# Optimization experiments

Hardware: AMD Instinct MI355X
Metric: run time of the kernel (lower is better)

The kernel has to match this reference:

```python
import jax, jax.numpy as jnp
import numpy as np

B, S, V, E, H, T = 256, 160, 50000, 300, 256, 200

def setup_inputs() -> dict:
    key = jax.random.key(0)
    ks = jax.random.split(key, 12)
    return {
        'x1': jax.random.randint(ks[0], (B, S), 0, V),
        'x2': jax.random.randint(ks[1], (B, S), 0, V),
        'x1mask': jnp.ones((B, S), jnp.float32),
        'key_c': jax.random.normal(ks[2], (B, S, T), jnp.float32) * 0.1,
        'key_r': jax.random.normal(ks[3], (B, S, T), jnp.float32) * 0.1,
        'emb_table': jax.random.normal(ks[4], (V, E), jnp.float32) * 0.1,
        'W_ih': jax.random.normal(ks[5], (4 * H, E), jnp.float32) * 0.05,
        'W_hh': jax.random.normal(ks[6], (4 * H, H), jnp.float32) * 0.05,
        'W_kh': jax.random.normal(ks[7], (4 * H, T), jnp.float32) * 0.05,
        'b_g': jnp.zeros((4 * H,), jnp.float32),
        'W_attn': jax.random.normal(ks[8], (H, H), jnp.float32) * 0.05,
        'b_attn': jnp.zeros((H,), jnp.float32),
        'M': jax.random.normal(ks[9], (H, H), jnp.float32) * 0.05,
        'b': jnp.zeros((1,), jnp.float32),
    }

def _run_rnn(x_emb, k_emb, W_ih, W_hh, W_kh, b_g):
    # x_emb: [B,S,E], k_emb: [B,S,T] -> hidden states [B,S,H]
    Bn = x_emb.shape[0]
    h0 = jnp.zeros((Bn, H), x_emb.dtype)
    c0 = jnp.zeros((Bn, H), x_emb.dtype)
    def cell(carry, inp):
        h, c = carry
        x_t, k_t = inp
        g = x_t @ W_ih.T + h @ W_hh.T + k_t @ W_kh.T + b_g  # [B,4H]
        i, f, gg, o = jnp.split(g, 4, axis=-1)
        c = jax.nn.sigmoid(f) * c + jax.nn.sigmoid(i) * jnp.tanh(gg)
        h = jax.nn.sigmoid(o) * jnp.tanh(c)
        return (h, c), h
    xs = (jnp.swapaxes(x_emb, 0, 1), jnp.swapaxes(k_emb, 0, 1))  # time-major
    (_, _), hs = jax.lax.scan(cell, (h0, c0), xs)
    return jnp.swapaxes(hs, 0, 1)  # [B,S,H]

def reference(x1, x2, x1mask, key_c, key_r, emb_table, W_ih, W_hh, W_kh, b_g,
              W_attn, b_attn, M, b):
    x1_emb = emb_table[x1]  # [B,S,E] (dropout = identity at eval)
    x2_emb = emb_table[x2]
    sc = _run_rnn(x1_emb, key_c, W_ih, W_hh, W_kh, b_g)  # context states [B,S,H]
    rs = _run_rnn(x2_emb, key_r, W_ih, W_hh, W_kh, b_g)
    r = rs[:, -1]  # last response hidden [B,H]
    # masked dot-product attention over context states keyed by r
    attn = sc @ W_attn.T + b_attn  # [B,S,H]
    energies = jnp.einsum('bsh,bh->bs', attn, r) * x1mask
    alpha = jax.nn.softmax(energies, axis=-1)
    c_attn = jnp.einsum('bs,bsh->bh', alpha, sc)
    # bilinear score
    o = jnp.einsum('bh,hk,bk->b', c_attn, M, r) + b[0]
    return o
```

## Files before the change

kernel.cpp:

```cpp
#include <hip/hip_runtime.h>
#include <math.h>

#define B_   256
#define S_   160
#define E_   300
#define H_   256
#define T_   200
#define G4H  1024
#define CH   16
#define NCH  10

typedef float  f32x4  __attribute__((ext_vector_type(4)));
typedef __bf16 bf16x4 __attribute__((ext_vector_type(4)));
typedef __bf16 bf16x8 __attribute__((ext_vector_type(8)));

__device__ __forceinline__ float sigf(float x) {
    float e = expf(-fabsf(x));
    float p = 1.0f / (1.0f + e);
    return x >= 0.0f ? p : e * p;
}

__device__ __forceinline__ int norig(int np) {
    return ((np >> 4) & 3) * 256 + ((np >> 6) << 4) + (np & 15);
}

__device__ __forceinline__ float4 pick4(const float* __restrict__ e,
                                        const float* __restrict__ k, int kg) {
    if (kg < E_)      return *(const float4*)(e + kg);
    if (kg < E_ + T_) return *(const float4*)(k + (kg - E_));
    return make_float4(0.f, 0.f, 0.f, 0.f);
}

__device__ __forceinline__ void split4(float4 v, bf16x4& h, bf16x4& l) {
    h[0] = (__bf16)v.x; l[0] = (__bf16)(v.x - (float)h[0]);
    h[1] = (__bf16)v.y; l[1] = (__bf16)(v.y - (float)h[1]);
    h[2] = (__bf16)v.z; l[2] = (__bf16)(v.z - (float)h[2]);
    h[3] = (__bf16)v.w; l[3] = (__bf16)(v.w - (float)h[3]);
}

__global__ __launch_bounds__(128) void prep_split(
    const float* __restrict__ Whh, const float* __restrict__ Wih,
    const float* __restrict__ Wkh,
    __bf16* __restrict__ whh_hi, __bf16* __restrict__ whh_lo,
    __bf16* __restrict__ wik_hi, __bf16* __restrict__ wik_lo)
{
    const int n  = blockIdx.x;
    const int np = ((n & 255) >> 4) * 64 + (n >> 8) * 16 + (n & 15);
    const int t  = threadIdx.x;
    {
        const int k4 = t * 4;
        float4 v;
        if (k4 < E_)            v = *(const float4*)(Wih + (size_t)n * E_ + k4);
        else if (k4 < E_ + T_)  v = *(const float4*)(Wkh + (size_t)n * T_ + (k4 - E_));
        else                    v = make_float4(0.f, 0.f, 0.f, 0.f);
        bf16x4 h, l;
        split4(v, h, l);
        *(bf16x4*)(wik_hi + (size_t)np * 512 + k4) = h;
        *(bf16x4*)(wik_lo + (size_t)np * 512 + k4) = l;
    }
    if (t < 64) {
        const int k4 = t * 4;
        const float4 v = *(const float4*)(Whh + (size_t)n * 256 + k4);
        bf16x4 h, l;
        split4(v, h, l);
        *(bf16x4*)(whh_hi + (size_t)np * 256 + k4) = h;
        *(bf16x4*)(whh_lo + (size_t)np * 256 + k4) = l;
    }
}

__global__ __launch_bounds__(256, 4) void gemm_g2(
    const int* __restrict__ x1, const int* __restrict__ x2,
    const float* __restrict__ key_c, const float* __restrict__ key_r,
    const float* __restrict__ emb,
    const __bf16* __restrict__ wik_hi, const __bf16* __restrict__ wik_lo,
    const float* __restrict__ bg,
    float* __restrict__ G, int s0)
{
    __shared__ __align__(16) __bf16 Ah[128 * 32];
    __shared__ __align__(16) __bf16 Al[128 * 32];
    __shared__ __align__(16) __bf16 Bh[128 * 32];
    __shared__ __align__(16) __bf16 Bl[128 * 32];

    const int t   = threadIdx.x;
    const int rnn = blockIdx.z;
    const int m0  = blockIdx.x * 128;
    const int n0  = blockIdx.y * 128;
    const int* xx = rnn ? x2 : x1;
    const float* key = rnn ? key_r : key_c;

    const int r0  = t >> 3;
    const int kq  = t & 7;
    const int csw = (((kq >> 1) ^ ((r0 >> 1) & 3)) * 16) + (kq & 1) * 8;

    const float* aeb[4]; const float* akb[4];
    const __bf16* wph[4]; const __bf16* wpl[4];
    #pragma unroll
    for (int i = 0; i < 4; ++i) {
        const int row = r0 + 32 * i;
        const int am  = m0 + row;
        const int bs  = (am >> 4) * S_ + s0 + (am & 15);
        aeb[i] = emb + (size_t)xx[bs] * E_;
        akb[i] = key + (size_t)bs * T_;
        wph[i] = wik_hi + (size_t)(n0 + row) * 512;
        wpl[i] = wik_lo + (size_t)(n0 + row) * 512;
    }

    const int w  = t >> 6;
    const int wm = w >> 1;
    const int wn = w & 1;
    const int l  = t & 63;
    const int cl = l & 15;
    const int ch = l >> 4;
    const int chs = ((ch ^ ((cl >> 1) & 3)) * 16);

    f32x4 acc[4][4];
    #pragma unroll
    for (int fm = 0; fm < 4; ++fm)
        #pragma unroll
        for (int fn = 0; fn < 4; ++fn) acc[fm][fn] = (f32x4){0.f, 0.f, 0.f, 0.f};

    for (int kt = 0; kt < 16; ++kt) {
        const int kg = kt * 32 + kq * 4;
        bf16x4 sAh[4], sAl[4], sBh[4], sBl[4];
        #pragma unroll
        for (int i = 0; i < 4; ++i) {
            const float4 va = pick4(aeb[i], akb[i], kg);
            split4(va, sAh[i], sAl[i]);
            sBh[i] = *(const bf16x4*)(wph[i] + kg);
            sBl[i] = *(const bf16x4*)(wpl[i] + kg);
        }
        __syncthreads();
        #pragma unroll
        for (int i = 0; i < 4; ++i) {
            const int off = (r0 + 32 * i) * 64 + csw;
            *(bf16x4*)((char*)Ah + off) = sAh[i];
            *(bf16x4*)((char*)Al + off) = sAl[i];
            *(bf16x4*)((char*)Bh + off) = sBh[i];
            *(bf16x4*)((char*)Bl + off) = sBl[i];
        }
        __syncthreads();

        bf16x8 fBh[4], fBl[4];
        #pragma unroll
        for (int fn = 0; fn < 4; ++fn) {
            const int off = (wn * 64 + fn * 16 + cl) * 64 + chs;
            fBh[fn] = *(const bf16x8*)((const char*)Bh + off);
            fBl[fn] = *(const bf16x8*)((const char*)Bl + off);
        }
        #pragma unroll
        for (int fm = 0; fm < 4; ++fm) {
            const int off = (wm * 64 + fm * 16 + cl) * 64 + chs;
            const bf16x8 fAh = *(const bf16x8*)((const char*)Ah + off);
            const bf16x8 fAl = *(const bf16x8*)((const char*)Al + off);
            #pragma unroll
            for (int fn = 0; fn < 4; ++fn) {
                acc[fm][fn] = __builtin_amdgcn_mfma_f32_16x16x32_bf16(fAh, fBh[fn], acc[fm][fn], 0, 0, 0);
                acc[fm][fn] = __builtin_amdgcn_mfma_f32_16x16x32_bf16(fAh, fBl[fn], acc[fm][fn], 0, 0, 0);
                acc[fm][fn] = __builtin_amdgcn_mfma_f32_16x16x32_bf16(fAl, fBh[fn], acc[fm][fn], 0, 0, 0);
            }
        }
    }

    float bgl[4];
    #pragma unroll
    for (int fn = 0; fn < 4; ++fn) bgl[fn] = bg[norig(n0 + wn * 64 + fn * 16 + cl)];

    #pragma unroll
    for (int fm = 0; fm < 4; ++fm) {
        #pragma unroll
        for (int r = 0; r < 4; ++r) {
            const int m  = m0 + wm * 64 + fm * 16 + ch * 4 + r;
            const int b  = m >> 4;
            const int sl = m & 15;
            float* rowp = G + ((size_t)(rnn * CH + sl) * B_ + b) * G4H;
            #pragma unroll
            for (int fn = 0; fn < 4; ++fn)
                rowp[n0 + wn * 64 + fn * 16 + cl] = acc[fm][fn][r] + bgl[fn];
        }
    }
}

__global__ __launch_bounds__(256, 2) void lstm_ks(
    const float* __restrict__ G,
    const __bf16* __restrict__ Whi, const __bf16* __restrict__ Wlo,
    const __bf16* __restrict__ hhi_in, const __bf16* __restrict__ hlo_in,
    __bf16* __restrict__ hhi_out, __bf16* __restrict__ hlo_out,
    float* __restrict__ cst, float* __restrict__ sc,
    int sl, int s_glob, int first)
{
    __shared__ float ps[64 * 66];

    const int t  = threadIdx.x;
    const int w  = t >> 6;
    const int l  = t & 63;
    const int cl = l & 15;
    const int ch = l >> 4;
    const int mt = blockIdx.x;
    const int jt = blockIdx.y;
    const int rnn = mt >> 4;
    const int b0  = (mt & 15) * 16;
    const int m0  = mt * 16;

    const int me = t >> 4;
    const int jl = t & 15;
    const int j  = jt * 16 + jl;
    float Ge[4];
    const float* Gb = G + ((size_t)(rnn * CH + sl) * B_ + b0 + me) * G4H + jt * 64;
    #pragma unroll
    for (int g = 0; g < 4; ++g) Ge[g] = Gb[g * 16 + jl];
    const float c_in = first ? 0.f : cst[(size_t)(m0 + me) * 256 + j];

    const size_t ab = (size_t)(m0 + cl) * 256 + w * 64 + ch * 8;
    const bf16x8 fAh0 = *(const bf16x8*)(hhi_in + ab);
    const bf16x8 fAh1 = *(const bf16x8*)(hhi_in + ab + 32);
    const bf16x8 fAl0 = *(const bf16x8*)(hlo_in + ab);
    const bf16x8 fAl1 = *(const bf16x8*)(hlo_in + ab + 32);

    bf16x8 fBh[4][2], fBl[4][2];
    #pragma unroll
    for (int g = 0; g < 4; ++g) {
        const size_t bb = (size_t)(jt * 64 + g * 16 + cl) * 256 + w * 64 + ch * 8;
        fBh[g][0] = *(const bf16x8*)(Whi + bb);
        fBh[g][1] = *(const bf16x8*)(Whi + bb + 32);
        fBl[g][0] = *(const bf16x8*)(Wlo + bb);
        fBl[g][1] = *(const bf16x8*)(Wlo + bb + 32);
    }

    f32x4 acc[4];
    #pragma unroll
    for (int g = 0; g < 4; ++g) acc[g] = (f32x4){0.f, 0.f, 0.f, 0.f};
    #pragma unroll
    for (int g = 0; g < 4; ++g) {
        acc[g] = __builtin_amdgcn_mfma_f32_16x16x32_bf16(fAh0, fBh[g][0], acc[g], 0, 0, 0);
        acc[g] = __builtin_amdgcn_mfma_f32_16x16x32_bf16(fAh1, fBh[g][1], acc[g], 0, 0, 0);
        acc[g] = __builtin_amdgcn_mfma_f32_16x16x32_bf16(fAh0, fBl[g][0], acc[g], 0, 0, 0);
        acc[g] = __builtin_amdgcn_mfma_f32_16x16x32_bf16(fAh1, fBl[g][1], acc[g], 0, 0, 0);
        acc[g] = __builtin_amdgcn_mfma_f32_16x16x32_bf16(fAl0, fBh[g][0], acc[g], 0, 0, 0);
        acc[g] = __builtin_amdgcn_mfma_f32_16x16x32_bf16(fAl1, fBh[g][1], acc[g], 0, 0, 0);
    }

    #pragma unroll
    for (int g = 0; g < 4; ++g)
        #pragma unroll
        for (int r = 0; r < 4; ++r)
            ps[(w * 16 + ch * 4 + r) * 66 + g * 16 + cl] = acc[g][r];
    __syncthreads();

    float g4[4];
    #pragma unroll
    for (int g = 0; g < 4; ++g) {
        float s = Ge[g];
        #pragma unroll
        for (int w2 = 0; w2 < 4; ++w2)
            s += ps[(w2 * 16 + me) * 66 + g * 16 + jl];
        g4[g] = s;
    }
    const float c = sigf(g4[1]) * c_in + sigf(g4[0]) * tanhf(g4[2]);
    const float h = sigf(g4[3]) * tanhf(c);
    cst[(size_t)(m0 + me) * 256 + j] = c;
    const __bf16 hh = (__bf16)h;
    const size_t ho = (size_t)(m0 + me) * 256 + j;
    hhi_out[ho] = hh;
    hlo_out[ho] = (__bf16)(h - (float)hh);
    if (rnn == 0)
        sc[((size_t)(b0 + me) * S_ + s_glob) * H_ + j] = h;
}

__global__ __launch_bounds__(256) void final_kernel(
    const float* __restrict__ sc,
    const __bf16* __restrict__ rhi, const __bf16* __restrict__ rlo,
    const float* __restrict__ Wattn, const float* __restrict__ battn,
    const float* __restrict__ M, const float* __restrict__ bscal,
    const float* __restrict__ mask, float* __restrict__ out)
{
    __shared__ float rs[256], us[256], red[256], as_[256];
    const int b = blockIdx.x;
    const int t = threadIdx.x;

    const size_t ri = (size_t)(256 + b) * 256 + t;
    rs[t] = (float)rhi[ri] + (float)rlo[ri];
    __syncthreads();

    float acc = 0.0f;
    for (int h = 0; h < 256; ++h) acc += rs[h] * Wattn[h * 256 + t];
    us[t] = acc;

    red[t] = battn[t] * rs[t];
    __syncthreads();
    for (int off = 128; off; off >>= 1) {
        if (t < off) red[t] += red[t + off];
        __syncthreads();
    }
    float beta = red[0];
    __syncthreads();

    float vh = 0.0f;
    {
        const float* Mrow = M + t * 256;
        for (int k = 0; k < 256; ++k) vh += Mrow[k] * rs[k];
    }

    float e = -INFINITY;
    if (t < S_) {
        float d = 0.0f;
        const float* scrow = sc + ((size_t)b * S_ + t) * H_;
        for (int h = 0; h < 256; ++h) d += scrow[h] * us[h];
        e = (d + beta) * mask[b * S_ + t];
    }
    red[t] = e;
    __syncthreads();
    for (int off = 128; off; off >>= 1) {
        if (t < off) red[t] = fmaxf(red[t], red[t + off]);
        __syncthreads();
    }
    float mx = red[0];
    __syncthreads();

    float p = (t < S_) ? expf(e - mx) : 0.0f;
    as_[t] = p;
    red[t] = p;
    __syncthreads();
    for (int off = 128; off; off >>= 1) {
        if (t < off) red[t] += red[t + off];
        __syncthreads();
    }
    float inv = 1.0f / red[0];
    __syncthreads();

    float ca = 0.0f;
    for (int s = 0; s < S_; ++s) ca += as_[s] * sc[((size_t)b * S_ + s) * H_ + t];
    ca *= inv;

    red[t] = ca * vh;
    __syncthreads();
    for (int off = 128; off; off >>= 1) {
        if (t < off) red[t] += red[t + off];
        __syncthreads();
    }
    if (t == 0) out[b] = red[0] + bscal[0];
}

extern "C" void kernel_launch(void* const* d_in, const int* in_sizes, int n_in,
                              void* d_out, int out_size, void* d_ws, size_t ws_size,
                              hipStream_t stream)
{
    const int*   x1    = (const int*)d_in[0];
    const int*   x2    = (const int*)d_in[1];
    const float* mask  = (const float*)d_in[2];
    const float* key_c = (const float*)d_in[3];
    const float* key_r = (const float*)d_in[4];
    const float* emb   = (const float*)d_in[5];
    const float* Wih   = (const float*)d_in[6];
    const float* Whh   = (const float*)d_in[7];
    const float* Wkh   = (const float*)d_in[8];
    const float* bg    = (const float*)d_in[9];
    const float* Wattn = (const float*)d_in[10];
    const float* battn = (const float*)d_in[11];
    const float* M     = (const float*)d_in[12];
    const float* bb    = (const float*)d_in[13];
    float* out = (float*)d_out;
    char*  wsb = (char*)d_ws;

    float*  G     = (float*)(wsb + 0);
    float*  sc    = (float*)(wsb + 33554432);
    __bf16* hhi0  = (__bf16*)(wsb + 75497472);
    __bf16* hlo0  = (__bf16*)(wsb + 75759616);
    __bf16* hhi1  = (__bf16*)(wsb + 76021760);
    __bf16* hlo1  = (__bf16*)(wsb + 76283904);
    float*  cst   = (float*)(wsb + 76546048);
    __bf16* WhhHi = (__bf16*)(wsb + 77070336);
    __bf16* WhhLo = (__bf16*)(wsb + 77594624);
    __bf16* WikHi = (__bf16*)(wsb + 78118912);
    __bf16* WikLo = (__bf16*)(wsb + 79167488);
    if (ws_size < 80216064) return;

    hipMemsetAsync(hhi0, 0, 524288, stream);
    prep_split<<<dim3(1024), 128, 0, stream>>>(Whh, Wih, Wkh,
                                               WhhHi, WhhLo, WikHi, WikLo);

    for (int ci = 0; ci < NCH; ++ci) {
        gemm_g2<<<dim3(32, 8, 2), 256, 0, stream>>>(x1, x2, key_c, key_r, emb,
                                                    WikHi, WikLo, bg, G, ci * CH);
        for (int slq = 0; slq < CH; ++slq) {
            const int s   = ci * CH + slq;
            const int par = s & 1;
            lstm_ks<<<dim3(32, 16), 256, 0, stream>>>(G, WhhHi, WhhLo,
                                                      par ? hhi1 : hhi0,
                                                      par ? hlo1 : hlo0,
                                                      par ? hhi0 : hhi1,
                                                      par ? hlo0 : hlo1,
                                                      cst, sc, slq, s, s == 0);
        }
    }

    final_kernel<<<dim3(256), 256, 0, stream>>>(sc, hhi0, hlo0, Wattn, battn,
                                                M, bb, mask, out);
}
```

Measured before the change: 1.603 ms.

## Double threads per block in input GEMM and LSTM step kernels

Both the chunked input-projection GEMM and the per-step recurrent LSTM kernel now launch 512 threads per block instead of 256. In the GEMM, each wave covers a 64x32 output subtile and each thread stages one row with 8-wide loads. In the LSTM step, the K=256 reduction is split across 8 waves of 32 instead of 4 waves of 64, with a larger shared partial-sum buffer, and only the first 256 threads run the gate nonlinearities. The aim is more waves in flight and shorter per-wave MFMA chains on the latency-bound recurrent step, at the cost of more shared-memory reduction work and half the threads idling in the epilogue.

```diff
diff --git a/kernel.cpp b/kernel.cpp
--- a/kernel.cpp
+++ b/kernel.cpp
@@ -68,7 +68,7 @@
     }
 }
 
-__global__ __launch_bounds__(256, 4) void gemm_g2(
+__global__ __launch_bounds__(512, 2) void gemm_g2(
     const int* __restrict__ x1, const int* __restrict__ x2,
     const float* __restrict__ key_c, const float* __restrict__ key_r,
     const float* __restrict__ emb,
@@ -88,62 +88,60 @@
     const int* xx = rnn ? x2 : x1;
     const float* key = rnn ? key_r : key_c;
 
-    const int r0  = t >> 3;
-    const int kq  = t & 7;
-    const int csw = (((kq >> 1) ^ ((r0 >> 1) & 3)) * 16) + (kq & 1) * 8;
-
-    const float* aeb[4]; const float* akb[4];
-    const __bf16* wph[4]; const __bf16* wpl[4];
-    #pragma unroll
-    for (int i = 0; i < 4; ++i) {
-        const int row = r0 + 32 * i;
-        const int am  = m0 + row;
-        const int bs  = (am >> 4) * S_ + s0 + (am & 15);
-        aeb[i] = emb + (size_t)xx[bs] * E_;
-        akb[i] = key + (size_t)bs * T_;
-        wph[i] = wik_hi + (size_t)(n0 + row) * 512;
-        wpl[i] = wik_lo + (size_t)(n0 + row) * 512;
+    const int r0 = t >> 2;
+    const int cq = t & 3;
+    const int csw = ((cq ^ ((r0 >> 1) & 3)) * 16);
+
+    const float* aeb; const float* akb;
+    const __bf16* wph; const __bf16* wpl;
+    {
+        const int am = m0 + r0;
+        const int bs = (am >> 4) * S_ + s0 + (am & 15);
+        aeb = emb + (size_t)xx[bs] * E_;
+        akb = key + (size_t)bs * T_;
+        wph = wik_hi + (size_t)(n0 + r0) * 512;
+        wpl = wik_lo + (size_t)(n0 + r0) * 512;
     }
 
     const int w  = t >> 6;
-    const int wm = w >> 1;
-    const int wn = w & 1;
+    const int wm = w >> 2;
+    const int wn = w & 3;
     const int l  = t & 63;
     const int cl = l & 15;
     const int ch = l >> 4;
     const int chs = ((ch ^ ((cl >> 1) & 3)) * 16);
 
-    f32x4 acc[4][4];
+    f32x4 acc[4][2];
     #pragma unroll
     for (int fm = 0; fm < 4; ++fm)
         #pragma unroll
-        for (int fn = 0; fn < 4; ++fn) acc[fm][fn] = (f32x4){0.f, 0.f, 0.f, 0.f};
+        for (int fn = 0; fn < 2; ++fn) acc[fm][fn] = (f32x4){0.f, 0.f, 0.f, 0.f};
 
     for (int kt = 0; kt < 16; ++kt) {
-        const int kg = kt * 32 + kq * 4;
-        bf16x4 sAh[4], sAl[4], sBh[4], sBl[4];
-        #pragma unroll
-        for (int i = 0; i < 4; ++i) {
-            const float4 va = pick4(aeb[i], akb[i], kg);
-            split4(va, sAh[i], sAl[i]);
-            sBh[i] = *(const bf16x4*)(wph[i] + kg);
-            sBl[i] = *(const bf16x4*)(wpl[i] + kg);
-        }
-        __syncthreads();
-        #pragma unroll
-        for (int i = 0; i < 4; ++i) {
-            const int off = (r0 + 32 * i) * 64 + csw;
-            *(bf16x4*)((char*)Ah + off) = sAh[i];
-            *(bf16x4*)((char*)Al + off) = sAl[i];
-            *(bf16x4*)((char*)Bh + off) = sBh[i];
-            *(bf16x4*)((char*)Bl + off) = sBl[i];
-        }
-        __syncthreads();
-
-        bf16x8 fBh[4], fBl[4];
-        #pragma unroll
-        for (int fn = 0; fn < 4; ++fn) {
-            const int off = (wn * 64 + fn * 16 + cl) * 64 + chs;
+        const int kg = kt * 32 + cq * 8;
+        const float4 va0 = pick4(aeb, akb, kg);
+        const float4 va1 = pick4(aeb, akb, kg + 4);
+        const bf16x8 vbh = *(const bf16x8*)(wph + kg);
+        const bf16x8 vbl = *(const bf16x8*)(wpl + kg);
+        bf16x4 h0, l0, h1, l1;
+        split4(va0, h0, l0);
+        split4(va1, h1, l1);
+        const bf16x8 sah = __builtin_shufflevector(h0, h1, 0, 1, 2, 3, 4, 5, 6, 7);
+        const bf16x8 sal = __builtin_shufflevector(l0, l1, 0, 1, 2, 3, 4, 5, 6, 7);
+        __syncthreads();
+        {
+            const int off = r0 * 64 + csw;
+            *(bf16x8*)((char*)Ah + off) = sah;
+            *(bf16x8*)((char*)Al + off) = sal;
+            *(bf16x8*)((char*)Bh + off) = vbh;
+            *(bf16x8*)((char*)Bl + off) = vbl;
+        }
+        __syncthreads();
+
+        bf16x8 fBh[2], fBl[2];
+        #pragma unroll
+        for (int fn = 0; fn < 2; ++fn) {
+            const int off = (wn * 32 + fn * 16 + cl) * 64 + chs;
             fBh[fn] = *(const bf16x8*)((const char*)Bh + off);
             fBl[fn] = *(const bf16x8*)((const char*)Bl + off);
         }
@@ -153,7 +151,7 @@
             const bf16x8 fAh = *(const bf16x8*)((const char*)Ah + off);
             const bf16x8 fAl = *(const bf16x8*)((const char*)Al + off);
             #pragma unroll
-            for (int fn = 0; fn < 4; ++fn) {
+            for (int fn = 0; fn < 2; ++fn) {
                 acc[fm][fn] = __builtin_amdgcn_mfma_f32_16x16x32_bf16(fAh, fBh[fn], acc[fm][fn], 0, 0, 0);
                 acc[fm][fn] = __builtin_amdgcn_mfma_f32_16x16x32_bf16(fAh, fBl[fn], acc[fm][fn], 0, 0, 0);
                 acc[fm][fn] = __builtin_amdgcn_mfma_f32_16x16x32_bf16(fAl, fBh[fn], acc[fm][fn], 0, 0, 0);
@@ -161,9 +159,10 @@
         }
     }
 
-    float bgl[4];
-    #pragma unroll
-    for (int fn = 0; fn < 4; ++fn) bgl[fn] = bg[norig(n0 + wn * 64 + fn * 16 + cl)];
+    float bgl[2];
+    #pragma unroll
+    for (int fn = 0; fn < 2; ++fn)
+        bgl[fn] = bg[norig(n0 + wn * 32 + fn * 16 + cl)];
 
     #pragma unroll
     for (int fm = 0; fm < 4; ++fm) {
@@ -174,13 +173,13 @@
             const int sl = m & 15;
             float* rowp = G + ((size_t)(rnn * CH + sl) * B_ + b) * G4H;
             #pragma unroll
-            for (int fn = 0; fn < 4; ++fn)
-                rowp[n0 + wn * 64 + fn * 16 + cl] = acc[fm][fn][r] + bgl[fn];
-        }
-    }
-}
-
-__global__ __launch_bounds__(256, 2) void lstm_ks(
+            for (int fn = 0; fn < 2; ++fn)
+                rowp[n0 + wn * 32 + fn * 16 + cl] = acc[fm][fn][r] + bgl[fn];
+        }
+    }
+}
+
+__global__ __launch_bounds__(512, 2) void lstm_ks(
     const float* __restrict__ G,
     const __bf16* __restrict__ Whi, const __bf16* __restrict__ Wlo,
     const __bf16* __restrict__ hhi_in, const __bf16* __restrict__ hlo_in,
@@ -188,7 +187,7 @@
     float* __restrict__ cst, float* __restrict__ sc,
     int sl, int s_glob, int first)
 {
-    __shared__ float ps[64 * 66];
+    __shared__ float ps[128 * 66];
 
     const int t  = threadIdx.x;
     const int w  = t >> 6;
@@ -201,29 +200,28 @@
     const int b0  = (mt & 15) * 16;
     const int m0  = mt * 16;
 
-    const int me = t >> 4;
+    const int me = (t >> 4) & 15;
     const int jl = t & 15;
     const int j  = jt * 16 + jl;
     float Ge[4];
-    const float* Gb = G + ((size_t)(rnn * CH + sl) * B_ + b0 + me) * G4H + jt * 64;
-    #pragma unroll
-    for (int g = 0; g < 4; ++g) Ge[g] = Gb[g * 16 + jl];
-    const float c_in = first ? 0.f : cst[(size_t)(m0 + me) * 256 + j];
-
-    const size_t ab = (size_t)(m0 + cl) * 256 + w * 64 + ch * 8;
-    const bf16x8 fAh0 = *(const bf16x8*)(hhi_in + ab);
-    const bf16x8 fAh1 = *(const bf16x8*)(hhi_in + ab + 32);
-    const bf16x8 fAl0 = *(const bf16x8*)(hlo_in + ab);
-    const bf16x8 fAl1 = *(const bf16x8*)(hlo_in + ab + 32);
-
-    bf16x8 fBh[4][2], fBl[4][2];
+    float c_in = 0.f;
+    if (t < 256) {
+        const float* Gb = G + ((size_t)(rnn * CH + sl) * B_ + b0 + me) * G4H + jt * 64;
+        #pragma unroll
+        for (int g = 0; g < 4; ++g) Ge[g] = Gb[g * 16 + jl];
+        if (!first) c_in = cst[(size_t)(m0 + me) * 256 + j];
+    }
+
+    const size_t ab = (size_t)(m0 + cl) * 256 + w * 32 + ch * 8;
+    const bf16x8 fAh = *(const bf16x8*)(hhi_in + ab);
+    const bf16x8 fAl = *(const bf16x8*)(hlo_in + ab);
+
+    bf16x8 fBh[4], fBl[4];
     #pragma unroll
     for (int g = 0; g < 4; ++g) {
-        const size_t bb = (size_t)(jt * 64 + g * 16 + cl) * 256 + w * 64 + ch * 8;
-        fBh[g][0] = *(const bf16x8*)(Whi + bb);
-        fBh[g][1] = *(const bf16x8*)(Whi + bb + 32);
-        fBl[g][0] = *(const bf16x8*)(Wlo + bb);
-        fBl[g][1] = *(const bf16x8*)(Wlo + bb + 32);
+        const size_t bb = (size_t)(jt * 64 + g * 16 + cl) * 256 + w * 32 + ch * 8;
+        fBh[g] = *(const bf16x8*)(Whi + bb);
+        fBl[g] = *(const bf16x8*)(Wlo + bb);
     }
 
     f32x4 acc[4];
@@ -231,12 +229,9 @@
     for (int g = 0; g < 4; ++g) acc[g] = (f32x4){0.f, 0.f, 0.f, 0.f};
     #pragma unroll
     for (int g = 0; g < 4; ++g) {
-        acc[g] = __builtin_amdgcn_mfma_f32_16x16x32_bf16(fAh0, fBh[g][0], acc[g], 0, 0, 0);
-        acc[g] = __builtin_amdgcn_mfma_f32_16x16x32_bf16(fAh1, fBh[g][1], acc[g], 0, 0, 0);
-        acc[g] = __builtin_amdgcn_mfma_f32_16x16x32_bf16(fAh0, fBl[g][0], acc[g], 0, 0, 0);
-        acc[g] = __builtin_amdgcn_mfma_f32_16x16x32_bf16(fAh1, fBl[g][1], acc[g], 0, 0, 0);
-        acc[g] = __builtin_amdgcn_mfma_f32_16x16x32_bf16(fAl0, fBh[g][0], acc[g], 0, 0, 0);
-        acc[g] = __builtin_amdgcn_mfma_f32_16x16x32_bf16(fAl1, fBh[g][1], acc[g], 0, 0, 0);
+        acc[g] = __builtin_amdgcn_mfma_f32_16x16x32_bf16(fAh, fBh[g], acc[g], 0, 0, 0);
+        acc[g] = __builtin_amdgcn_mfma_f32_16x16x32_bf16(fAh, fBl[g], acc[g], 0, 0, 0);
+        acc[g] = __builtin_amdgcn_mfma_f32_16x16x32_bf16(fAl, fBh[g], acc[g], 0, 0, 0);
     }
 
     #pragma unroll
@@ -246,24 +241,26 @@
             ps[(w * 16 + ch * 4 + r) * 66 + g * 16 + cl] = acc[g][r];
     __syncthreads();
 
-    float g4[4];
-    #pragma unroll
-    for (int g = 0; g < 4; ++g) {
-        float s = Ge[g];
-        #pragma unroll
-        for (int w2 = 0; w2 < 4; ++w2)
-            s += ps[(w2 * 16 + me) * 66 + g * 16 + jl];
-        g4[g] = s;
-    }
-    const float c = sigf(g4[1]) * c_in + sigf(g4[0]) * tanhf(g4[2]);
-    const float h = sigf(g4[3]) * tanhf(c);
-    cst[(size_t)(m0 + me) * 256 + j] = c;
-    const __bf16 hh = (__bf16)h;
-    const size_t ho = (size_t)(m0 + me) * 256 + j;
-    hhi_out[ho] = hh;
-    hlo_out[ho] = (__bf16)(h - (float)hh);
-    if (rnn == 0)
-        sc[((size_t)(b0 + me) * S_ + s_glob) * H_ + j] = h;
+    if (t < 256) {
+        float g4[4];
+        #pragma unroll
+        for (int g = 0; g < 4; ++g) {
+            float s = Ge[g];
+            #pragma unroll
+            for (int w2 = 0; w2 < 8; ++w2)
+                s += ps[(w2 * 16 + me) * 66 + g * 16 + jl];
+            g4[g] = s;
+        }
+        const float c = sigf(g4[1]) * c_in + sigf(g4[0]) * tanhf(g4[2]);
+        const float h = sigf(g4[3]) * tanhf(c);
+        cst[(size_t)(m0 + me) * 256 + j] = c;
+        const __bf16 hh = (__bf16)h;
+        const size_t ho = (size_t)(m0 + me) * 256 + j;
+        hhi_out[ho] = hh;
+        hlo_out[ho] = (__bf16)(h - (float)hh);
+        if (rnn == 0)
+            sc[((size_t)(b0 + me) * S_ + s_glob) * H_ + j] = h;
+    }
 }
 
 __global__ __launch_bounds__(256) void final_kernel(
@@ -379,12 +376,12 @@
                                                WhhHi, WhhLo, WikHi, WikLo);
 
     for (int ci = 0; ci < NCH; ++ci) {
-        gemm_g2<<<dim3(32, 8, 2), 256, 0, stream>>>(x1, x2, key_c, key_r, emb,
+        gemm_g2<<<dim3(32, 8, 2), 512, 0, stream>>>(x1, x2, key_c, key_r, emb,
                                                     WikHi, WikLo, bg, G, ci * CH);
         for (int slq = 0; slq < CH; ++slq) {
             const int s   = ci * CH + slq;
             const int par = s & 1;
-            lstm_ks<<<dim3(32, 16), 256, 0, stream>>>(G, WhhHi, WhhLo,
+            lstm_ks<<<dim3(32, 16), 512, 0, stream>>>(G, WhhHi, WhhLo,
                                                       par ? hhi1 : hhi0,
                                                       par ? hlo1 : hlo0,
                                                       par ? hhi0 : hhi1,
```

New measurement: 1.508 ms. -5.9%, faster.
